# Performance work log

Hardware: AMD Instinct MI355X
Metric: run time of the kernel (lower is better)

The kernel has to match this reference:

```python
import jax, jax.numpy as jnp
import numpy as np

D_MODEL = 1024
NUM_HEADS = 16
HEAD_DIM = D_MODEL // NUM_HEADS


def setup_inputs() -> dict:
    key = jax.random.key(0)
    ks = jax.random.split(key, 11)
    B, S, D = 2, 2048, D_MODEL
    scale = 1.0 / np.sqrt(D)
    inp = {
        "query": jax.random.normal(ks[0], (B, S, D), jnp.float32),
        "key": jax.random.normal(ks[1], (B, S, D), jnp.float32),
        "value": jax.random.normal(ks[2], (B, S, D), jnp.float32),
        "Wq": jax.random.normal(ks[3], (D, D), jnp.float32) * scale,
        "bq": jnp.zeros((D,), jnp.float32),
        "Wk": jax.random.normal(ks[4], (D, D), jnp.float32) * scale,
        "bk": jnp.zeros((D,), jnp.float32),
        "Wv": jax.random.normal(ks[5], (D, D), jnp.float32) * scale,
        "bv": jnp.zeros((D,), jnp.float32),
        "Wo": jax.random.normal(ks[6], (D, D), jnp.float32) * scale,
        "bo": jnp.zeros((D,), jnp.float32),
    }
    return inp


def reference(query, key, value, Wq, bq, Wk, bk, Wv, bv, Wo, bo):
    B, S, D = query.shape
    H, hd = NUM_HEADS, HEAD_DIM
    # linear projections (x @ W^T + b, torch nn.Linear convention)
    Q = query @ Wq.T + bq
    K = key @ Wk.T + bk
    V = value @ Wv.T + bv
    # split heads: [B, S, H, hd] -> [B, H, S, hd]
    Q = Q.reshape(B, S, H, hd).transpose(0, 2, 1, 3)
    K = K.reshape(B, S, H, hd).transpose(0, 2, 1, 3)
    V = V.reshape(B, S, H, hd).transpose(0, 2, 1, 3)
    # scaled dot-product attention (explicit, non-flash)
    scores = jnp.einsum("bhqd,bhkd->bhqk", Q, K) / jnp.sqrt(jnp.float32(hd)).astype(Q.dtype)
    attn = jax.nn.softmax(scores, axis=-1)
    out = jnp.einsum("bhqk,bhkd->bhqd", attn, V)
    # merge heads: [B, H, S, hd] -> [B, S, D]
    out = out.transpose(0, 2, 1, 3).reshape(B, S, D)
    return out @ Wo.T + bo
```

## Files before the change

kernel.cpp:

```cpp
#include <hip/hip_runtime.h>
#include <hip/hip_bf16.h>


constexpr int D_MODEL = 1024;
constexpr int S_LEN   = 2048;
constexpr int BATCH   = 2;
constexpr int NH      = 16;
constexpr int HD      = 64;
constexpr int ROWS    = BATCH * S_LEN;

typedef __attribute__((ext_vector_type(8))) short short8;
typedef __attribute__((ext_vector_type(4))) float float4a;

static __device__ __forceinline__ unsigned short f2bf(float f) {
  union { float f; unsigned u; } v{f};
  unsigned r = v.u + 0x7FFFu + ((v.u >> 16) & 1u);
  return (unsigned short)(r >> 16);
}

static __device__ __forceinline__ unsigned pack_bf16(float a, float b) {
#if __has_builtin(__builtin_amdgcn_cvt_pk_bf16_f32)
  typedef __attribute__((ext_vector_type(2))) __bf16 bf16x2;
  union { bf16x2 v; unsigned u; } c;
  c.v = __builtin_amdgcn_cvt_pk_bf16_f32(a, b);
  return c.u;
#else
  return (unsigned)f2bf(a) | ((unsigned)f2bf(b) << 16);
#endif
}

static __device__ __forceinline__ float bf2f(unsigned short u) {
  union { unsigned u; float f; } v;
  v.u = (unsigned)u << 16;
  return v.f;
}

static __device__ __forceinline__ void async16(const void* g, void* l) {
  __builtin_amdgcn_global_load_lds(
      (const __attribute__((address_space(1))) unsigned int*)g,
      (__attribute__((address_space(3))) unsigned int*)l, 16, 0, 0);
}

struct ConvArgs { const float* s[7]; unsigned short* d[7]; int n[7]; };

__global__ __launch_bounds__(256) void convert_bf16(ConvArgs a) {
  const int which = blockIdx.y;
  const int i = (blockIdx.x * 256 + threadIdx.x) * 8;
  if (i >= a.n[which]) return;
  const float4* s = (const float4*)(a.s[which] + i);
  float4 x = s[0], y = s[1];
  unsigned t[4] = {pack_bf16(x.x, x.y), pack_bf16(x.z, x.w),
                   pack_bf16(y.x, y.y), pack_bf16(y.z, y.w)};
  *(short8*)(a.d[which] + i) = *(short8*)t;
}

template <int MODE>
static __device__ __forceinline__ void gemm_body(
    const unsigned short* __restrict__ A, const unsigned short* __restrict__ W,
    const float* __restrict__ bias, void* __restrict__ Yv, float scale,
    unsigned short* As, unsigned short* Bs, unsigned short* Tb) {
  const int tid = threadIdx.x;
  const int w = tid >> 6, lane = tid & 63;
  const int l15 = lane & 15, quad = lane >> 4;
  const int row0 = blockIdx.x * 128, col0 = blockIdx.y * 128;
  const int wm = (w & 1) * 64, wn = (w >> 1) * 64;

  float4a acc[4][4];
#pragma unroll
  for (int i = 0; i < 4; i++)
#pragma unroll
    for (int j = 0; j < 4; j++) acc[i][j] = (float4a){0.f, 0.f, 0.f, 0.f};

  const int swA = (quad + (wm >> 1) + (l15 >> 1)) & 3;
  const int swB = (quad + (wn >> 1) + (l15 >> 1)) & 3;

  for (int kt = 0; kt < D_MODEL; kt += 32) {
    __syncthreads();
#pragma unroll
    for (int j = 0; j < 2; j++) {
      const int i = w * 2 + j;
      const int r = i * 16 + (lane >> 2);
      const int c = ((lane & 3) - (r >> 1)) & 3;
      async16(W + (size_t)(col0 + r) * D_MODEL + kt + c * 8, (char*)Bs + i * 1024);
      async16(A + (size_t)(row0 + r) * D_MODEL + kt + c * 8, (char*)As + i * 1024);
    }
    __syncthreads();

    short8 af[4], bf[4];
#pragma unroll
    for (int mt = 0; mt < 4; mt++) {
      const int r = wm + mt * 16 + l15;
      af[mt] = *(const short8*)&As[(r * 4 + swA) * 8];
    }
#pragma unroll
    for (int nt = 0; nt < 4; nt++) {
      const int r = wn + nt * 16 + l15;
      bf[nt] = *(const short8*)&Bs[(r * 4 + swB) * 8];
    }
#pragma unroll
    for (int mt = 0; mt < 4; mt++)
#pragma unroll
      for (int nt = 0; nt < 4; nt++)
        acc[mt][nt] = __builtin_amdgcn_mfma_f32_16x16x32_bf16(af[mt], bf[nt], acc[mt][nt], 0, 0, 0);
  }

  int cols[4];
  float bvs[4];
#pragma unroll
  for (int nt = 0; nt < 4; nt++) {
    cols[nt] = col0 + wn + nt * 16 + l15;
    bvs[nt]  = bias[cols[nt]] * ((MODE == 0) ? scale : 1.0f);
  }

  if constexpr (MODE == 0) {
    unsigned short* Y = (unsigned short*)Yv;
#pragma unroll
    for (int mt = 0; mt < 4; mt++)
#pragma unroll
      for (int r = 0; r < 4; r++) {
        const int m = row0 + wm + mt * 16 + quad * 4 + r;
        const int bb = m >> 11, s = m & 2047;
#pragma unroll
        for (int nt = 0; nt < 4; nt++) {
          const int h = cols[nt] >> 6, d = cols[nt] & 63;
          Y[(((size_t)(bb * NH + h)) * S_LEN + s) * HD + d] =
              f2bf(acc[mt][nt][r] * scale + bvs[nt]);
        }
      }
  } else {
    __syncthreads();
    unsigned short* T = Tb + w * (64 * 32);
    unsigned short* Y = (unsigned short*)Yv;
#pragma unroll
    for (int p = 0; p < 2; p++) {
      if (p) { asm volatile("s_waitcnt lgkmcnt(0)" ::: "memory"); }
#pragma unroll
      for (int mi = 0; mi < 2; mi++) {
        const int mt = 2 * p + mi;
#pragma unroll
        for (int r = 0; r < 4; r++) {
          const int sl = mi * 16 + quad * 4 + r;
          const int cch = sl >> 3;
#pragma unroll
          for (int nt = 0; nt < 4; nt++) {
            const int dl = nt * 16 + l15;
            const int slot = cch ^ (dl & 3);
            T[dl * 32 + slot * 8 + (sl & 7)] = f2bf(acc[mt][nt][r] + bvs[nt]);
          }
        }
      }
      asm volatile("s_waitcnt lgkmcnt(0)" ::: "memory");
#pragma unroll
      for (int j = 0; j < 4; j++) {
        const int cid = j * 64 + lane;
        const int dl = cid >> 2;
        const int c  = cid & 3;
        const int slot = c ^ (dl & 3);
        short8 v = *(const short8*)&T[dl * 32 + slot * 8];
        const int col = col0 + wn + dl;
        const int h = col >> 6, d = col & 63;
        const int m = row0 + wm + p * 32 + c * 8;
        const int bb = m >> 11, s = m & 2047;
        *(short8*)&Y[(((size_t)(bb * NH + h)) * HD + d) * S_LEN + s] = v;
      }
    }
  }
}

__global__ __launch_bounds__(256) void gemm_qkv(
    const unsigned short* xq, const unsigned short* xk, const unsigned short* xv,
    const unsigned short* wq, const unsigned short* wk, const unsigned short* wv,
    const float* bq, const float* bk, const float* bv,
    unsigned short* Q, unsigned short* K, unsigned short* Vt) {
  __shared__ unsigned short smem[2 * 128 * 32];
  unsigned short* As = smem;
  unsigned short* Bs = smem + 128 * 32;
  unsigned short* Tb = smem;
  const int z = blockIdx.z;
  if (z == 0)      gemm_body<0>(xq, wq, bq, Q,  0.125f * 1.44269504f, As, Bs, Tb);
  else if (z == 1) gemm_body<0>(xk, wk, bk, K,  1.0f, As, Bs, Tb);
  else             gemm_body<2>(xv, wv, bv, Vt, 1.0f, As, Bs, Tb);
}

__global__ __launch_bounds__(256) void gemm_o(
    const unsigned short* __restrict__ Op, const float* __restrict__ Lp,
    const unsigned short* __restrict__ wo, const float* __restrict__ bo,
    float* __restrict__ out) {
  __shared__ unsigned short As[64 * 32];
  __shared__ unsigned short Bs[128 * 32];
  const int tid = threadIdx.x;
  const int w = tid >> 6, lane = tid & 63;
  const int l15 = lane & 15, quad = lane >> 4;
  const int row0 = blockIdx.x * 64, col0 = blockIdx.y * 128;
  const int wn = w * 32;

  const int ar = w * 16 + (lane >> 2);
  const int cg = lane & 3;
  const int asl = (cg + (ar >> 1)) & 3;
  const int grow = row0 + ar;
  const unsigned short* P0 = Op + (size_t)grow * D_MODEL + cg * 8;
  const unsigned short* P1 = P0 + (size_t)ROWS * D_MODEL;
  const float* L0 = Lp + (size_t)grow * NH;
  const float* L1 = L0 + (size_t)ROWS * NH;

  float4a acc[4][2];
#pragma unroll
  for (int i = 0; i < 4; i++)
#pragma unroll
    for (int j = 0; j < 2; j++) acc[i][j] = (float4a){0.f, 0.f, 0.f, 0.f};

  const int swA = (quad + (l15 >> 1)) & 3;
  const int swB = (quad + (wn >> 1) + (l15 >> 1)) & 3;

  for (int kt = 0; kt < D_MODEL; kt += 32) {
    const int h = kt >> 6;
    const float rinv = 1.0f / (L0[h] + L1[h]);
    short8 a = *(const short8*)(P0 + kt);
    short8 b = *(const short8*)(P1 + kt);
    unsigned t[4];
#pragma unroll
    for (int i = 0; i < 4; i++) {
      const float v0 = (bf2f((unsigned short)a[2 * i]) + bf2f((unsigned short)b[2 * i])) * rinv;
      const float v1 = (bf2f((unsigned short)a[2 * i + 1]) + bf2f((unsigned short)b[2 * i + 1])) * rinv;
      t[i] = pack_bf16(v0, v1);
    }
    __syncthreads();
    *(short8*)&As[(ar * 4 + asl) * 8] = *(short8*)t;
#pragma unroll
    for (int j = 0; j < 2; j++) {
      const int i = w * 2 + j;
      const int r = i * 16 + (lane >> 2);
      const int c = ((lane & 3) - (r >> 1)) & 3;
      async16(wo + (size_t)(col0 + r) * D_MODEL + kt + c * 8, (char*)Bs + i * 1024);
    }
    __syncthreads();

    short8 af[4], bf[2];
#pragma unroll
    for (int mt = 0; mt < 4; mt++) {
      const int r = mt * 16 + l15;
      af[mt] = *(const short8*)&As[(r * 4 + swA) * 8];
    }
#pragma unroll
    for (int nt = 0; nt < 2; nt++) {
      const int r = wn + nt * 16 + l15;
      bf[nt] = *(const short8*)&Bs[(r * 4 + swB) * 8];
    }
#pragma unroll
    for (int mt = 0; mt < 4; mt++)
#pragma unroll
      for (int nt = 0; nt < 2; nt++)
        acc[mt][nt] = __builtin_amdgcn_mfma_f32_16x16x32_bf16(af[mt], bf[nt], acc[mt][nt], 0, 0, 0);
  }

#pragma unroll
  for (int nt = 0; nt < 2; nt++) {
    const int col = col0 + wn + nt * 16 + l15;
    const float bv = bo[col];
#pragma unroll
    for (int mt = 0; mt < 4; mt++)
#pragma unroll
      for (int r = 0; r < 4; r++) {
        const int m = row0 + mt * 16 + quad * 4 + r;
        out[(size_t)m * D_MODEL + col] = acc[mt][nt][r] + bv;
      }
  }
}

__global__ __launch_bounds__(256) void attn_kernel(
    const unsigned short* __restrict__ Qh, const unsigned short* __restrict__ Kh,
    const unsigned short* __restrict__ Vt, unsigned short* __restrict__ Op,
    float* __restrict__ Lp) {
  const int n   = blockIdx.x;
  const int idx = n >> 3;
  const int qb  = idx & 15;
  const int g   = (n & 7) + 8 * (idx >> 4);
  const int h   = g & 15;
  const int z   = g >> 4;
  const int bb  = z >> 1, sp = z & 1;

  const int tid = threadIdx.x;
  const int w = tid >> 6, lane = tid & 63;
  const int l15 = lane & 15, quad = lane >> 4;

  __shared__ unsigned short Ks[64 * 64];
  __shared__ unsigned short Vs[64 * 64];
  __shared__ unsigned short Ps[4][32][72];

  const size_t bh = (size_t)(bb * NH + h);
  const unsigned short* Qp = Qh + bh * S_LEN * HD;
  const unsigned short* Kp = Kh + bh * S_LEN * HD;
  const unsigned short* Vp = Vt + bh * (size_t)HD * S_LEN;

  short8 qf[2][2];
#pragma unroll
  for (int qnt = 0; qnt < 2; qnt++)
#pragma unroll
    for (int c = 0; c < 2; c++)
      qf[qnt][c] = *(const short8*)(Qp + (size_t)(qb * 128 + w * 32 + qnt * 16 + l15) * HD +
                                    c * 32 + quad * 8);

  unsigned short ob[8] = {0x3F80, 0x3F80, 0x3F80, 0x3F80, 0x3F80, 0x3F80, 0x3F80, 0x3F80};
  const short8 ones = *(short8*)ob;

  float4a Oacc[2][4];
#pragma unroll
  for (int a = 0; a < 2; a++)
#pragma unroll
    for (int b = 0; b < 4; b++) Oacc[a][b] = (float4a){0.f, 0.f, 0.f, 0.f};
  float4a Lacc[2] = {(float4a){0.f, 0.f, 0.f, 0.f}, (float4a){0.f, 0.f, 0.f, 0.f}};

  const int sw0 = (quad + l15) & 7;
  const int sw1 = (quad + 4 + l15) & 7;

  for (int kb = sp * 1024; kb < sp * 1024 + 1024; kb += 64) {
    __syncthreads();
#pragma unroll
    for (int j = 0; j < 2; j++) {
      const int i = w * 2 + j;
      const int r = i * 8 + (lane >> 3);
      const int c = ((lane & 7) - r) & 7;
      async16(Kp + (size_t)(kb + r) * HD + c * 8, (char*)Ks + i * 1024);
      async16(Vp + (size_t)r * S_LEN + kb + c * 8, (char*)Vs + i * 1024);
    }
    __syncthreads();

#pragma unroll
    for (int mt = 0; mt < 4; mt++) {
      const int rb = (mt * 16 + l15) * 8;
      short8 a0 = *(const short8*)&Ks[(rb + sw0) * 8];
      short8 a1 = *(const short8*)&Ks[(rb + sw1) * 8];
#pragma unroll
      for (int qnt = 0; qnt < 2; qnt++) {
        float4a s = (float4a){0.f, 0.f, 0.f, 0.f};
        s = __builtin_amdgcn_mfma_f32_16x16x32_bf16(a0, qf[qnt][0], s, 0, 0, 0);
        s = __builtin_amdgcn_mfma_f32_16x16x32_bf16(a1, qf[qnt][1], s, 0, 0, 0);
        uint2 pk;
        pk.x = pack_bf16(__builtin_amdgcn_exp2f(s[0]), __builtin_amdgcn_exp2f(s[1]));
        pk.y = pack_bf16(__builtin_amdgcn_exp2f(s[2]), __builtin_amdgcn_exp2f(s[3]));
        *(uint2*)&Ps[w][qnt * 16 + l15][mt * 16 + quad * 4] = pk;
      }
    }
    asm volatile("s_waitcnt lgkmcnt(0)" ::: "memory");

#pragma unroll
    for (int c = 0; c < 2; c++) {
      short8 pa0 = *(const short8*)&Ps[w][l15][c * 32 + quad * 8];
      short8 pa1 = *(const short8*)&Ps[w][16 + l15][c * 32 + quad * 8];
      Lacc[0] = __builtin_amdgcn_mfma_f32_16x16x32_bf16(pa0, ones, Lacc[0], 0, 0, 0);
      Lacc[1] = __builtin_amdgcn_mfma_f32_16x16x32_bf16(pa1, ones, Lacc[1], 0, 0, 0);
      const int vsw = (c * 4 + quad + l15) & 7;
#pragma unroll
      for (int nt = 0; nt < 4; nt++) {
        short8 vb = *(const short8*)&Vs[((nt * 16 + l15) * 8 + vsw) * 8];
        Oacc[0][nt] = __builtin_amdgcn_mfma_f32_16x16x32_bf16(pa0, vb, Oacc[0][nt], 0, 0, 0);
        Oacc[1][nt] = __builtin_amdgcn_mfma_f32_16x16x32_bf16(pa1, vb, Oacc[1][nt], 0, 0, 0);
      }
    }
  }

  if (l15 == 0) {
#pragma unroll
    for (int qnt = 0; qnt < 2; qnt++)
#pragma unroll
      for (int reg = 0; reg < 4; reg++) {
        const int q = qb * 128 + w * 32 + qnt * 16 + quad * 4 + reg;
        Lp[(size_t)sp * ROWS * NH + ((size_t)bb * S_LEN + q) * NH + h] = Lacc[qnt][reg];
      }
  }

  unsigned short* Ob = Op + (size_t)sp * ROWS * D_MODEL;
#pragma unroll
  for (int qnt = 0; qnt < 2; qnt++) {
#pragma unroll
    for (int reg = 0; reg < 4; reg++) {
      const int q = qb * 128 + w * 32 + qnt * 16 + quad * 4 + reg;
      unsigned short* orow = Ob + ((size_t)bb * S_LEN + q) * D_MODEL + h * HD;
#pragma unroll
      for (int nt = 0; nt < 4; nt++)
        orow[nt * 16 + l15] = f2bf(Oacc[qnt][nt][reg]);
    }
  }
}

extern "C" void kernel_launch(void* const* d_in, const int* in_sizes, int n_in,
                              void* d_out, int out_size, void* d_ws, size_t ws_size,
                              hipStream_t stream) {
  const float* query = (const float*)d_in[0];
  const float* key   = (const float*)d_in[1];
  const float* value = (const float*)d_in[2];
  const float* Wq = (const float*)d_in[3];
  const float* bq = (const float*)d_in[4];
  const float* Wk = (const float*)d_in[5];
  const float* bk = (const float*)d_in[6];
  const float* Wv = (const float*)d_in[7];
  const float* bv = (const float*)d_in[8];
  const float* Wo = (const float*)d_in[9];
  const float* bo = (const float*)d_in[10];
  float* out = (float*)d_out;

  char* ws = (char*)d_ws;
  const size_t MB = 1024 * 1024;
  unsigned short* xq16 = (unsigned short*)(ws + 0 * MB);
  unsigned short* xk16 = (unsigned short*)(ws + 8 * MB);
  unsigned short* xv16 = (unsigned short*)(ws + 16 * MB);
  unsigned short* wq16 = (unsigned short*)(ws + 24 * MB);
  unsigned short* wk16 = (unsigned short*)(ws + 26 * MB);
  unsigned short* wv16 = (unsigned short*)(ws + 28 * MB);
  unsigned short* qbuf  = (unsigned short*)(ws + 32 * MB);
  unsigned short* kbuf  = (unsigned short*)(ws + 40 * MB);
  unsigned short* vtbuf = (unsigned short*)(ws + 48 * MB);
  unsigned short* wo16  = (unsigned short*)(ws + 56 * MB);
  float* Lp = (float*)(ws + 58 * MB);
  unsigned short* Op = (unsigned short*)(ws + 0 * MB);

  ConvArgs ca;
  const int NX = ROWS * D_MODEL, NW = D_MODEL * D_MODEL;
  ca.s[0] = query; ca.d[0] = xq16; ca.n[0] = NX;
  ca.s[1] = key;   ca.d[1] = xk16; ca.n[1] = NX;
  ca.s[2] = value; ca.d[2] = xv16; ca.n[2] = NX;
  ca.s[3] = Wq;    ca.d[3] = wq16; ca.n[3] = NW;
  ca.s[4] = Wk;    ca.d[4] = wk16; ca.n[4] = NW;
  ca.s[5] = Wv;    ca.d[5] = wv16; ca.n[5] = NW;
  ca.s[6] = Wo;    ca.d[6] = wo16; ca.n[6] = NW;
  hipLaunchKernelGGL(convert_bf16, dim3(NX / 2048, 7), dim3(256), 0, stream, ca);

  dim3 gqkv(ROWS / 128, D_MODEL / 128, 3);
  hipLaunchKernelGGL(gemm_qkv, gqkv, dim3(256), 0, stream,
                     xq16, xk16, xv16, wq16, wk16, wv16, bq, bk, bv,
                     qbuf, kbuf, vtbuf);

  hipLaunchKernelGGL(attn_kernel, dim3(1024), dim3(256), 0, stream,
                     qbuf, kbuf, vtbuf, Op, Lp);

  dim3 go(ROWS / 64, D_MODEL / 128);
  hipLaunchKernelGGL(gemm_o, go, dim3(256), 0, stream, Op, Lp, wo16, bo, out);
}
```

Measured before the change: 236.5 us.

## Prefetch next K/V tile into registers while computing current tile

Replaces the synchronous async global-to-LDS copy of each K/V tile with a register double-buffer: the next tile's K and V are loaded into registers while the current tile is processed, then written to shared memory at the top of the next iteration. Global pointer arithmetic is hoisted out of the loop. This aims to hide global load latency behind the MFMA/softmax work, at the cost of extra VGPRs and explicit waitcnt/barrier sequencing that may reduce occupancy.

Result: no change. 237.3 us (+0.3%).

```diff
diff --git a/kernel.cpp b/kernel.cpp
--- a/kernel.cpp
+++ b/kernel.cpp
@@ -292,6 +292,17 @@
   const unsigned short* Kp = Kh + bh * S_LEN * HD;
   const unsigned short* Vp = Vt + bh * (size_t)HD * S_LEN;
 
+  const int r0 = w * 16 + (lane >> 3);
+  const int c0 = ((lane & 7) - r0) & 7;
+  const unsigned short* Kg0 = Kp + (size_t)r0 * HD + c0 * 8;
+  const unsigned short* Kg1 = Kg0 + 8 * HD;
+  const unsigned short* Vg0 = Vp + (size_t)r0 * S_LEN + c0 * 8;
+  const unsigned short* Vg1 = Vg0 + 8 * S_LEN;
+  unsigned short* Kd0 = (unsigned short*)((char*)Ks + (w * 2) * 1024 + (size_t)lane * 16);
+  unsigned short* Kd1 = (unsigned short*)((char*)Kd0 + 1024);
+  unsigned short* Vd0 = (unsigned short*)((char*)Vs + (w * 2) * 1024 + (size_t)lane * 16);
+  unsigned short* Vd1 = (unsigned short*)((char*)Vd0 + 1024);
+
   short8 qf[2][2];
 #pragma unroll
   for (int qnt = 0; qnt < 2; qnt++)
@@ -313,17 +324,32 @@
   const int sw0 = (quad + l15) & 7;
   const int sw1 = (quad + 4 + l15) & 7;
 
-  for (int kb = sp * 1024; kb < sp * 1024 + 1024; kb += 64) {
-    __syncthreads();
-#pragma unroll
-    for (int j = 0; j < 2; j++) {
-      const int i = w * 2 + j;
-      const int r = i * 8 + (lane >> 3);
-      const int c = ((lane & 7) - r) & 7;
-      async16(Kp + (size_t)(kb + r) * HD + c * 8, (char*)Ks + i * 1024);
-      async16(Vp + (size_t)r * S_LEN + kb + c * 8, (char*)Vs + i * 1024);
-    }
-    __syncthreads();
+  const int kb0 = sp * 1024, kbend = kb0 + 1024;
+
+  short8 kr0 = *(const short8*)(Kg0 + (size_t)kb0 * HD);
+  short8 kr1 = *(const short8*)(Kg1 + (size_t)kb0 * HD);
+  short8 vr0 = *(const short8*)(Vg0 + kb0);
+  short8 vr1 = *(const short8*)(Vg1 + kb0);
+
+  for (int kb = kb0; kb < kbend; kb += 64) {
+    asm volatile("s_waitcnt lgkmcnt(0)" ::: "memory");
+    __builtin_amdgcn_sched_barrier(0);
+    __builtin_amdgcn_s_barrier();
+    asm volatile("s_waitcnt vmcnt(0)" ::: "memory");
+    __builtin_amdgcn_sched_barrier(0);
+    *(short8*)Kd0 = kr0;
+    *(short8*)Kd1 = kr1;
+    *(short8*)Vd0 = vr0;
+    *(short8*)Vd1 = vr1;
+    if (kb + 64 < kbend) {
+      kr0 = *(const short8*)(Kg0 + (size_t)(kb + 64) * HD);
+      kr1 = *(const short8*)(Kg1 + (size_t)(kb + 64) * HD);
+      vr0 = *(const short8*)(Vg0 + (kb + 64));
+      vr1 = *(const short8*)(Vg1 + (kb + 64));
+    }
+    asm volatile("s_waitcnt lgkmcnt(0)" ::: "memory");
+    __builtin_amdgcn_sched_barrier(0);
+    __builtin_amdgcn_s_barrier();
 
 #pragma unroll
     for (int mt = 0; mt < 4; mt++) {
```
